# Optimization experiments

Measured on AMD Instinct MI355X. Metric: run time of the kernel, lower is better.

Reference implementation:

```python
import jax, jax.numpy as jnp
import numpy as np

B, C, H, W = 32, 512, 56, 56
GROUPS = 32
CG = C // GROUPS  # channels per group = 16
EPS = 1e-5


def setup_inputs() -> dict:
    key = jax.random.key(0)
    ks = jax.random.split(key, 5)
    return {
        "x": jax.random.normal(ks[0], (B, C, H, W), jnp.float32),
        "w1": jax.random.normal(ks[1], (CG, CG), jnp.float32) * 0.1,   # conv1x1 weight [out,in]
        "b1": jax.random.normal(ks[2], (CG,), jnp.float32) * 0.1,
        "w3": jax.random.normal(ks[3], (CG, CG, 3, 3), jnp.float32) * 0.05,  # conv3x3 OIHW
        "b3": jax.random.normal(ks[4], (CG,), jnp.float32) * 0.1,
        "gn_w": jnp.ones((CG,), jnp.float32),
        "gn_b": jnp.zeros((CG,), jnp.float32),
    }


def reference(x, w1, b1, w3, b3, gn_w, gn_b):
    b, c, h, w = x.shape
    bg = b * GROUPS
    gx = x.reshape(bg, CG, h, w)                                  # group_x
    # directional pooling
    x_h = gx.mean(axis=3, keepdims=True)                          # [bg,cg,h,1]
    x_w = gx.mean(axis=2, keepdims=True).transpose(0, 1, 3, 2)    # [bg,cg,w,1]
    y = jnp.concatenate([x_h, x_w], axis=2)                       # [bg,cg,h+w,1]
    # conv1x1 == channel mixing
    y = jnp.einsum('oc,bcld->bold', w1, y) + b1[None, :, None, None]
    xh = jax.nn.sigmoid(y[:, :, :h])                              # [bg,cg,h,1]
    xw = jax.nn.sigmoid(y[:, :, h:].transpose(0, 1, 3, 2))        # [bg,cg,1,w]
    # GroupNorm(num_groups=cg, num_channels=cg) == per-channel instance norm
    x1 = gx * xh * xw
    mu = x1.mean(axis=(2, 3), keepdims=True)
    var = x1.var(axis=(2, 3), keepdims=True)
    x1 = (x1 - mu) * jax.lax.rsqrt(var + EPS) * gn_w[None, :, None, None] + gn_b[None, :, None, None]
    # conv3x3 branch
    x2 = jax.lax.conv_general_dilated(
        gx, w3, (1, 1), 'SAME',
        dimension_numbers=('NCHW', 'OIHW', 'NCHW')) + b3[None, :, None, None]
    # cross attention weights
    a1 = jax.nn.softmax(x1.mean(axis=(2, 3)), axis=-1)            # [bg,cg]
    a2 = jax.nn.softmax(x2.mean(axis=(2, 3)), axis=-1)            # [bg,cg]
    x1f = x1.reshape(bg, CG, h * w)
    x2f = x2.reshape(bg, CG, h * w)
    out1 = jnp.einsum('bc,bcl->bl', a1, x2f)                      # [bg,hw]
    out2 = jnp.einsum('bc,bcl->bl', a2, x1f)                      # [bg,hw]
    weights = (out1 + out2).reshape(bg, 1, h, w)
    out = gx * jax.nn.sigmoid(weights)
    return out.reshape(b, c, h, w)
```

## Files before the change

### kernel.cpp

```cpp
#include <hip/hip_runtime.h>
#include <math.h>

#define GROUPS 32
#define CG 16
#define HH 56
#define WW 56
#define HW (HH*WW)
#define BG 1024
#define EPS 1e-5f

#define RB 4
#define NB 14
#define NR (RB+2)
#define LROW 60
#define CPAD 4
#define CSTR (NR*LROW+CPAD)
#define XWS 60
#define GHS 9

__global__ __launch_bounds__(256) void kA(const float* __restrict__ x,
        const float* __restrict__ w1, const float* __restrict__ b1,
        const float* __restrict__ w3, const float* __restrict__ b3,
        const float* __restrict__ gn_w, const float* __restrict__ gn_b,
        float* __restrict__ ws_xh, float* __restrict__ ws_xw,
        float* __restrict__ ws_asc, float* __restrict__ ws_aofs,
        float* __restrict__ ws_wa)
{
    const int g = blockIdx.x;
    const int tid = threadIdx.x;
    const float* gx = x + (size_t)g * CG * HW;

    __shared__ float s_row[CG][HH];
    __shared__ float s_col[CG][WW];
    __shared__ float s_xh[CG][HH];
    __shared__ float s_xw[CG][WW];
    __shared__ float s_st[CG][9];
    __shared__ float s_x2p[CG][CG];
    __shared__ float ls1[CG], ls2[CG];

    if (g == 0 && tid < CG * 9 + 1) {
        float m = gn_b[0];
        #pragma unroll
        for (int c = 1; c < CG; ++c) m = fmaxf(m, gn_b[c]);
        float a1[CG]; float den = 0.f;
        #pragma unroll
        for (int c = 0; c < CG; ++c) { a1[c] = __expf(gn_b[c] - m); den += a1[c]; }
        float inv = 1.f / den;
        if (tid < CG * 9) {
            int ci = tid / 9, k = tid - (tid / 9) * 9;
            float s = 0.f;
            #pragma unroll
            for (int o = 0; o < CG; ++o) s += a1[o] * w3[(size_t)(o * CG + ci) * 9 + k];
            ws_wa[tid] = s * inv;
        } else {
            float s = 0.f;
            #pragma unroll
            for (int o = 0; o < CG; ++o) s += a1[o] * b3[o];
            ws_wa[CG * 9] = s * inv;
        }
    }

    {
        const int grp = tid >> 4;
        const int q   = tid & 15;
        const float* pc = gx + grp * HW;
        float c0 = 0.f, c1 = 0.f, c2 = 0.f, c3 = 0.f;
        #pragma unroll 4
        for (int row = 0; row < HH; ++row) {
            float4 v = make_float4(0.f, 0.f, 0.f, 0.f);
            if (q < 14) v = *(const float4*)(pc + row * WW + q * 4);
            c0 += v.x; c1 += v.y; c2 += v.z; c3 += v.w;
            float rs = (v.x + v.y) + (v.z + v.w);
            rs += __shfl_down(rs, 8);
            rs += __shfl_down(rs, 4);
            rs += __shfl_down(rs, 2);
            rs += __shfl_down(rs, 1);
            if (q == 0) s_row[grp][row] = rs * (1.0f / WW);
        }
        if (q < 14) {
            s_col[grp][q * 4 + 0] = c0 * (1.0f / HH);
            s_col[grp][q * 4 + 1] = c1 * (1.0f / HH);
            s_col[grp][q * 4 + 2] = c2 * (1.0f / HH);
            s_col[grp][q * 4 + 3] = c3 * (1.0f / HH);
        }
    }
    __syncthreads();

    for (int t = tid; t < 2 * CG * HH; t += 256) {
        int hpart = (t < CG * HH);
        int tt = hpart ? t : t - CG * HH;
        int o = tt / HH, i = tt - (tt / HH) * HH;
        float v = b1[o];
        #pragma unroll
        for (int c = 0; c < CG; ++c)
            v += w1[o * CG + c] * (hpart ? s_row[c][i] : s_col[c][i]);
        float sg = 1.f / (1.f + __expf(-v));
        if (hpart) { s_xh[o][i] = sg; ws_xh[(size_t)g * CG * HH + tt] = sg; }
        else       { s_xw[o][i] = sg; ws_xw[(size_t)g * CG * WW + tt] = sg; }
    }

    if (tid < CG) {
        const int c = tid;
        float S = 0.f;
        #pragma unroll
        for (int r = 0; r < HH; ++r) S += s_row[c][r];
        s_st[c][0] = S * (float)WW;
        s_st[c][1] = (float)WW * s_row[c][HH - 1];
        s_st[c][2] = (float)WW * s_row[c][0];
        s_st[c][3] = (float)HH * s_col[c][WW - 1];
        s_st[c][4] = (float)HH * s_col[c][0];
        const float* p = gx + c * HW;
        s_st[c][5] = p[0];
        s_st[c][6] = p[WW - 1];
        s_st[c][7] = p[(HH - 1) * WW];
        s_st[c][8] = p[(HH - 1) * WW + WW - 1];
    }
    __syncthreads();

    {
        const int o = tid >> 4, c = tid & 15;
        const float* wp = w3 + (size_t)(o * CG + c) * 9;
        const float* st = s_st[c];
        float S = st[0];
        float acc = 0.f;
        #pragma unroll
        for (int dy = 0; dy < 3; ++dy) {
            float Rv = (dy == 0) ? st[1] : (dy == 2 ? st[2] : 0.f);
            #pragma unroll
            for (int dx = 0; dx < 3; ++dx) {
                float Cv = (dx == 0) ? st[3] : (dx == 2 ? st[4] : 0.f);
                float T = S - Rv - Cv;
                if (dy != 1 && dx != 1)
                    T += (dy == 0) ? ((dx == 0) ? st[8] : st[7])
                                   : ((dx == 0) ? st[6] : st[5]);
                acc += wp[dy * 3 + dx] * T;
            }
        }
        s_x2p[c][o] = acc;
    }

    {
        const int c = tid >> 4;
        const int q = tid & 15;
        float s1 = 0.f, s2 = 0.f;
        if (q < 14) {
            const float* pc = gx + c * HW;
            float xw0 = s_xw[c][q * 4 + 0], xw1 = s_xw[c][q * 4 + 1];
            float xw2 = s_xw[c][q * 4 + 2], xw3v = s_xw[c][q * 4 + 3];
            #pragma unroll 4
            for (int row = 0; row < HH; ++row) {
                float4 v = *(const float4*)(pc + row * WW + q * 4);
                float xh = s_xh[c][row];
                float t0 = v.x * xh * xw0;
                float t1 = v.y * xh * xw1;
                float t2 = v.z * xh * xw2;
                float t3 = v.w * xh * xw3v;
                s1 += (t0 + t1) + (t2 + t3);
                s2 += (t0 * t0 + t1 * t1) + (t2 * t2 + t3 * t3);
            }
        }
        s1 += __shfl_down(s1, 8);  s2 += __shfl_down(s2, 8);
        s1 += __shfl_down(s1, 4);  s2 += __shfl_down(s2, 4);
        s1 += __shfl_down(s1, 2);  s2 += __shfl_down(s2, 2);
        s1 += __shfl_down(s1, 1);  s2 += __shfl_down(s2, 1);
        if (q == 0) { ls1[c] = s1; ls2[c] = s2; }
    }
    __syncthreads();

    if (tid < CG) {
        const int o = tid;
        float x2 = (float)HW * b3[o];
        #pragma unroll
        for (int c = 0; c < CG; ++c) x2 += s_x2p[c][o];

        float mu  = ls1[o] * (1.0f / HW);
        float var = ls2[o] * (1.0f / HW) - mu * mu;
        float sc  = gn_w[o] * rsqrtf(var + EPS);
        float sh  = gn_b[o] - mu * sc;

        float v2 = x2 * (1.0f / HW);
        float m = v2;
        #pragma unroll
        for (int off = 8; off; off >>= 1) m = fmaxf(m, __shfl_xor(m, off));
        float e = __expf(v2 - m);
        float den = e;
        #pragma unroll
        for (int off = 8; off; off >>= 1) den += __shfl_xor(den, off);
        float a2 = e / den;

        ws_asc[(size_t)g * CG + o] = a2 * sc;
        float part = a2 * sh;
        #pragma unroll
        for (int off = 8; off; off >>= 1) part += __shfl_xor(part, off);
        if (o == 0) ws_aofs[g] = part;
    }
}

__global__ __launch_bounds__(256, 4) void kBC(const float* __restrict__ x,
        const float* __restrict__ ws_xh, const float* __restrict__ ws_xw,
        const float* __restrict__ ws_asc, const float* __restrict__ ws_aofs,
        const float* __restrict__ ws_wa, float* __restrict__ out)
{
    const int g = blockIdx.x / NB;
    const int band = blockIdx.x - g * NB;
    const int y0 = band * RB;
    const int tid = threadIdx.x;
    const float* gx = x + (size_t)g * CG * HW;
    float* og = out + (size_t)g * CG * HW;

    __shared__ float s_in[CG * CSTR];
    __shared__ float s_xw[CG * XWS];
    __shared__ float s_gh[CG * GHS];
    __shared__ float s_wa[CG * 9];
    __shared__ float s_bias;

    if (tid < 96) {
        int c = tid / NR, r = tid - c * NR;
        *(float4*)&s_in[c * CSTR + r * LROW] = make_float4(0.f, 0.f, 0.f, 0.f);
    } else if (tid < 112) {
        int c = tid - 96;
        *(float4*)&s_in[c * CSTR + NR * LROW] = make_float4(0.f, 0.f, 0.f, 0.f);
    } else {
        s_wa[tid - 112] = ws_wa[tid - 112];
    }
    if (tid < CG * 14) {
        int c = tid / 14, q = tid - c * 14;
        *(float4*)&s_xw[c * XWS + 4 * q] =
            *(const float4*)&ws_xw[(size_t)g * CG * WW + c * WW + 4 * q];
    }
    if (tid < CG * RB) {
        int c = tid >> 2, r = tid & 3;
        s_gh[c * GHS + r] = ws_asc[(size_t)g * CG + c]
                          * ws_xh[(size_t)g * CG * HH + c * HH + y0 + r];
    }
    if (tid == 255) s_bias = ws_wa[CG * 9] + ws_aofs[0 + g];

    for (int t = tid; t < CG * NR * (WW / 4); t += 256) {
        int c = t / (NR * 14);
        int rem = t - c * (NR * 14);
        int r = rem / 14, q = rem - r * 14;
        int ry = y0 - 1 + r;
        float4 v = make_float4(0.f, 0.f, 0.f, 0.f);
        if (ry >= 0 && ry < HH)
            v = *(const float4*)(gx + c * HW + ry * WW + 4 * q);
        *(float4*)&s_in[c * CSTR + r * LROW + 4 + 4 * q] = v;
    }
    __syncthreads();

    if (tid < 224) {
        const int c   = tid & 15;
        const int sp  = tid >> 4;
        const int ypr = sp / 7;
        const int k   = sp - ypr * 7;
        const int x0  = 8 * k;

        float w[9];
        #pragma unroll
        for (int i = 0; i < 9; ++i) w[i] = s_wa[c * 9 + i];

        float4 X0 = *(const float4*)&s_xw[c * XWS + x0];
        float4 X1 = *(const float4*)&s_xw[c * XWS + x0 + 4];
        float gh0 = s_gh[c * GHS + 2 * ypr];
        float gh1 = s_gh[c * GHS + 2 * ypr + 1];
        float g0[8], g1[8];
        {
            float xwv[8] = {X0.x, X0.y, X0.z, X0.w, X1.x, X1.y, X1.z, X1.w};
            #pragma unroll
            for (int j = 0; j < 8; ++j) { g0[j] = gh0 * xwv[j]; g1[j] = gh1 * xwv[j]; }
        }

        float acc0[8], acc1[8];
        #pragma unroll
        for (int j = 0; j < 8; ++j) { acc0[j] = 0.f; acc1[j] = 0.f; }

        const int base = c * CSTR + 2 * ypr * LROW + x0;
        #pragma unroll
        for (int rr = 0; rr < 4; ++rr) {
            const float* rp = &s_in[base + rr * LROW];
            float4 R0 = *(const float4*)(rp);
            float4 R1 = *(const float4*)(rp + 4);
            float4 R2 = *(const float4*)(rp + 8);
            float4 R3 = *(const float4*)(rp + 12);
            float win[10] = {R0.w, R1.x, R1.y, R1.z, R1.w,
                             R2.x, R2.y, R2.z, R2.w, R3.x};
            if (rr < 3) {
                float a0 = w[3 * rr], a1 = w[3 * rr + 1], a2 = w[3 * rr + 2];
                #pragma unroll
                for (int j = 0; j < 8; ++j)
                    acc0[j] += a0 * win[j] + a1 * win[j + 1] + a2 * win[j + 2];
            }
            if (rr > 0) {
                float b0 = w[3 * (rr - 1)], b1 = w[3 * (rr - 1) + 1], b2 = w[3 * (rr - 1) + 2];
                #pragma unroll
                for (int j = 0; j < 8; ++j)
                    acc1[j] += b0 * win[j] + b1 * win[j + 1] + b2 * win[j + 2];
            }
            if (rr == 1) {
                #pragma unroll
                for (int j = 0; j < 8; ++j) acc0[j] += g0[j] * win[j + 1];
            }
            if (rr == 2) {
                #pragma unroll
                for (int j = 0; j < 8; ++j) acc1[j] += g1[j] * win[j + 1];
            }
        }

        #pragma unroll
        for (int m = 1; m <= 8; m <<= 1) {
            #pragma unroll
            for (int j = 0; j < 8; ++j) {
                acc0[j] += __shfl_xor(acc0[j], m);
                acc1[j] += __shfl_xor(acc1[j], m);
            }
        }

        float bias = s_bias;
        float sg0[8], sg1[8];
        #pragma unroll
        for (int j = 0; j < 8; ++j) {
            sg0[j] = 1.f / (1.f + __expf(-(acc0[j] + bias)));
            sg1[j] = 1.f / (1.f + __expf(-(acc1[j] + bias)));
        }

        const float* c0p = &s_in[base + 1 * LROW + 4];
        const float* c1p = &s_in[base + 2 * LROW + 4];
        float4 C00 = *(const float4*)(c0p);
        float4 C01 = *(const float4*)(c0p + 4);
        float4 C10 = *(const float4*)(c1p);
        float4 C11 = *(const float4*)(c1p + 4);

        float* o0 = og + c * HW + (y0 + 2 * ypr) * WW + x0;
        float* o1 = o0 + WW;
        *(float4*)(o0)     = make_float4(C00.x * sg0[0], C00.y * sg0[1],
                                         C00.z * sg0[2], C00.w * sg0[3]);
        *(float4*)(o0 + 4) = make_float4(C01.x * sg0[4], C01.y * sg0[5],
                                         C01.z * sg0[6], C01.w * sg0[7]);
        *(float4*)(o1)     = make_float4(C10.x * sg1[0], C10.y * sg1[1],
                                         C10.z * sg1[2], C10.w * sg1[3]);
        *(float4*)(o1 + 4) = make_float4(C11.x * sg1[4], C11.y * sg1[5],
                                         C11.z * sg1[6], C11.w * sg1[7]);
    }
}

extern "C" void kernel_launch(void* const* d_in, const int* in_sizes, int n_in,
                              void* d_out, int out_size, void* d_ws, size_t ws_size,
                              hipStream_t stream)
{
    const float* x    = (const float*)d_in[0];
    const float* w1   = (const float*)d_in[1];
    const float* b1   = (const float*)d_in[2];
    const float* w3   = (const float*)d_in[3];
    const float* b3   = (const float*)d_in[4];
    const float* gn_w = (const float*)d_in[5];
    const float* gn_b = (const float*)d_in[6];
    float* out = (float*)d_out;

    float* ws = (float*)d_ws;
    float* ws_xh   = ws;
    float* ws_xw   = ws_xh + (size_t)BG * CG * HH;
    float* ws_asc  = ws_xw + (size_t)BG * CG * WW;
    float* ws_aofs = ws_asc + (size_t)BG * CG;
    float* ws_wa   = ws_aofs + (size_t)BG;

    kA<<<BG, 256, 0, stream>>>(x, w1, b1, w3, b3, gn_w, gn_b,
                               ws_xh, ws_xw, ws_asc, ws_aofs, ws_wa);
    kBC<<<BG * NB, 256, 0, stream>>>(x, ws_xh, ws_xw, ws_asc, ws_aofs,
                                     ws_wa, out);
}
```

Measured before the change: 486.4 us.

## Fuse stats and output kernels into one block-per-group kernel looping over bands

Merges the statistics kernel and the banded conv/gating kernel into one kernel. Each block handles one group, keeps the pooled gates, attention scales and folded conv weights in shared memory, then loops over 14 row bands to produce the output. This removes the workspace round-trip and the second launch, and the group's re-read of x may hit cache. In exchange, the grid shrinks from about 14k blocks to 1024, and each band's load and compute are serialized by barriers with no overlap, which can hurt latency hiding.

Result: faster. 476.8 us (-2.0%).

```diff
diff --git a/kernel.cpp b/kernel.cpp
--- a/kernel.cpp
+++ b/kernel.cpp
@@ -16,29 +16,34 @@
 #define CPAD 4
 #define CSTR (NR*LROW+CPAD)
 #define XWS 60
-#define GHS 9
-
-__global__ __launch_bounds__(256) void kA(const float* __restrict__ x,
+#define XHS 57
+
+#define U_ROW 0
+#define U_COL 896
+#define U_ST  1792
+#define U_X2P 1936
+#define U_LS1 2192
+#define U_LS2 2208
+
+__global__ __launch_bounds__(256, 4) void kF(const float* __restrict__ x,
         const float* __restrict__ w1, const float* __restrict__ b1,
         const float* __restrict__ w3, const float* __restrict__ b3,
         const float* __restrict__ gn_w, const float* __restrict__ gn_b,
-        float* __restrict__ ws_xh, float* __restrict__ ws_xw,
-        float* __restrict__ ws_asc, float* __restrict__ ws_aofs,
-        float* __restrict__ ws_wa)
+        float* __restrict__ out)
 {
     const int g = blockIdx.x;
     const int tid = threadIdx.x;
     const float* gx = x + (size_t)g * CG * HW;
-
-    __shared__ float s_row[CG][HH];
-    __shared__ float s_col[CG][WW];
-    __shared__ float s_xh[CG][HH];
-    __shared__ float s_xw[CG][WW];
-    __shared__ float s_st[CG][9];
-    __shared__ float s_x2p[CG][CG];
-    __shared__ float ls1[CG], ls2[CG];
-
-    if (g == 0 && tid < CG * 9 + 1) {
+    float* og = out + (size_t)g * CG * HW;
+
+    __shared__ float s_u[CG * CSTR];
+    __shared__ float s_xh[CG * XHS];
+    __shared__ float s_xw[CG * XWS];
+    __shared__ float s_wa[CG * 9 + 1];
+    __shared__ float s_asc[CG];
+    __shared__ float s_bias;
+
+    if (tid < CG * 9 + 1) {
         float m = gn_b[0];
         #pragma unroll
         for (int c = 1; c < CG; ++c) m = fmaxf(m, gn_b[c]);
@@ -51,12 +56,12 @@
             float s = 0.f;
             #pragma unroll
             for (int o = 0; o < CG; ++o) s += a1[o] * w3[(size_t)(o * CG + ci) * 9 + k];
-            ws_wa[tid] = s * inv;
+            s_wa[tid] = s * inv;
         } else {
             float s = 0.f;
             #pragma unroll
             for (int o = 0; o < CG; ++o) s += a1[o] * b3[o];
-            ws_wa[CG * 9] = s * inv;
+            s_wa[CG * 9] = s * inv;
         }
     }
 
@@ -65,23 +70,32 @@
         const int q   = tid & 15;
         const float* pc = gx + grp * HW;
         float c0 = 0.f, c1 = 0.f, c2 = 0.f, c3 = 0.f;
-        #pragma unroll 4
-        for (int row = 0; row < HH; ++row) {
-            float4 v = make_float4(0.f, 0.f, 0.f, 0.f);
-            if (q < 14) v = *(const float4*)(pc + row * WW + q * 4);
-            c0 += v.x; c1 += v.y; c2 += v.z; c3 += v.w;
-            float rs = (v.x + v.y) + (v.z + v.w);
-            rs += __shfl_down(rs, 8);
-            rs += __shfl_down(rs, 4);
-            rs += __shfl_down(rs, 2);
-            rs += __shfl_down(rs, 1);
-            if (q == 0) s_row[grp][row] = rs * (1.0f / WW);
+        #pragma unroll 2
+        for (int row = 0; row < HH; row += 2) {
+            float4 va = make_float4(0.f, 0.f, 0.f, 0.f);
+            float4 vb = va;
+            if (q < 14) {
+                va = *(const float4*)(pc + row * WW + q * 4);
+                vb = *(const float4*)(pc + (row + 1) * WW + q * 4);
+            }
+            c0 += va.x + vb.x; c1 += va.y + vb.y;
+            c2 += va.z + vb.z; c3 += va.w + vb.w;
+            float ra = (va.x + va.y) + (va.z + va.w);
+            float rb = (vb.x + vb.y) + (vb.z + vb.w);
+            ra += __shfl_down(ra, 8);  rb += __shfl_down(rb, 8);
+            ra += __shfl_down(ra, 4);  rb += __shfl_down(rb, 4);
+            ra += __shfl_down(ra, 2);  rb += __shfl_down(rb, 2);
+            ra += __shfl_down(ra, 1);  rb += __shfl_down(rb, 1);
+            if (q == 0) {
+                s_u[U_ROW + grp * HH + row]     = ra * (1.0f / WW);
+                s_u[U_ROW + grp * HH + row + 1] = rb * (1.0f / WW);
+            }
         }
         if (q < 14) {
-            s_col[grp][q * 4 + 0] = c0 * (1.0f / HH);
-            s_col[grp][q * 4 + 1] = c1 * (1.0f / HH);
-            s_col[grp][q * 4 + 2] = c2 * (1.0f / HH);
-            s_col[grp][q * 4 + 3] = c3 * (1.0f / HH);
+            s_u[U_COL + grp * WW + q * 4 + 0] = c0 * (1.0f / HH);
+            s_u[U_COL + grp * WW + q * 4 + 1] = c1 * (1.0f / HH);
+            s_u[U_COL + grp * WW + q * 4 + 2] = c2 * (1.0f / HH);
+            s_u[U_COL + grp * WW + q * 4 + 3] = c3 * (1.0f / HH);
         }
     }
     __syncthreads();
@@ -93,34 +107,36 @@
         float v = b1[o];
         #pragma unroll
         for (int c = 0; c < CG; ++c)
-            v += w1[o * CG + c] * (hpart ? s_row[c][i] : s_col[c][i]);
+            v += w1[o * CG + c] * (hpart ? s_u[U_ROW + c * HH + i]
+                                         : s_u[U_COL + c * WW + i]);
         float sg = 1.f / (1.f + __expf(-v));
-        if (hpart) { s_xh[o][i] = sg; ws_xh[(size_t)g * CG * HH + tt] = sg; }
-        else       { s_xw[o][i] = sg; ws_xw[(size_t)g * CG * WW + tt] = sg; }
+        if (hpart) s_xh[o * XHS + i] = sg;
+        else       s_xw[o * XWS + i] = sg;
     }
 
     if (tid < CG) {
         const int c = tid;
         float S = 0.f;
         #pragma unroll
-        for (int r = 0; r < HH; ++r) S += s_row[c][r];
-        s_st[c][0] = S * (float)WW;
-        s_st[c][1] = (float)WW * s_row[c][HH - 1];
-        s_st[c][2] = (float)WW * s_row[c][0];
-        s_st[c][3] = (float)HH * s_col[c][WW - 1];
-        s_st[c][4] = (float)HH * s_col[c][0];
+        for (int r = 0; r < HH; ++r) S += s_u[U_ROW + c * HH + r];
+        float* st = &s_u[U_ST + c * 9];
+        st[0] = S * (float)WW;
+        st[1] = (float)WW * s_u[U_ROW + c * HH + HH - 1];
+        st[2] = (float)WW * s_u[U_ROW + c * HH];
+        st[3] = (float)HH * s_u[U_COL + c * WW + WW - 1];
+        st[4] = (float)HH * s_u[U_COL + c * WW];
         const float* p = gx + c * HW;
-        s_st[c][5] = p[0];
-        s_st[c][6] = p[WW - 1];
-        s_st[c][7] = p[(HH - 1) * WW];
-        s_st[c][8] = p[(HH - 1) * WW + WW - 1];
+        st[5] = p[0];
+        st[6] = p[WW - 1];
+        st[7] = p[(HH - 1) * WW];
+        st[8] = p[(HH - 1) * WW + WW - 1];
     }
     __syncthreads();
 
     {
         const int o = tid >> 4, c = tid & 15;
         const float* wp = w3 + (size_t)(o * CG + c) * 9;
-        const float* st = s_st[c];
+        const float* st = &s_u[U_ST + c * 9];
         float S = st[0];
         float acc = 0.f;
         #pragma unroll
@@ -136,7 +152,7 @@
                 acc += wp[dy * 3 + dx] * T;
             }
         }
-        s_x2p[c][o] = acc;
+        s_u[U_X2P + c * CG + o] = acc;
     }
 
     {
@@ -145,12 +161,12 @@
         float s1 = 0.f, s2 = 0.f;
         if (q < 14) {
             const float* pc = gx + c * HW;
-            float xw0 = s_xw[c][q * 4 + 0], xw1 = s_xw[c][q * 4 + 1];
-            float xw2 = s_xw[c][q * 4 + 2], xw3v = s_xw[c][q * 4 + 3];
+            float xw0 = s_xw[c * XWS + q * 4 + 0], xw1 = s_xw[c * XWS + q * 4 + 1];
+            float xw2 = s_xw[c * XWS + q * 4 + 2], xw3v = s_xw[c * XWS + q * 4 + 3];
             #pragma unroll 4
             for (int row = 0; row < HH; ++row) {
                 float4 v = *(const float4*)(pc + row * WW + q * 4);
-                float xh = s_xh[c][row];
+                float xh = s_xh[c * XHS + row];
                 float t0 = v.x * xh * xw0;
                 float t1 = v.y * xh * xw1;
                 float t2 = v.z * xh * xw2;
@@ -163,7 +179,7 @@
         s1 += __shfl_down(s1, 4);  s2 += __shfl_down(s2, 4);
         s1 += __shfl_down(s1, 2);  s2 += __shfl_down(s2, 2);
         s1 += __shfl_down(s1, 1);  s2 += __shfl_down(s2, 1);
-        if (q == 0) { ls1[c] = s1; ls2[c] = s2; }
+        if (q == 0) { s_u[U_LS1 + c] = s1; s_u[U_LS2 + c] = s2; }
     }
     __syncthreads();
 
@@ -171,10 +187,10 @@
         const int o = tid;
         float x2 = (float)HW * b3[o];
         #pragma unroll
-        for (int c = 0; c < CG; ++c) x2 += s_x2p[c][o];
-
-        float mu  = ls1[o] * (1.0f / HW);
-        float var = ls2[o] * (1.0f / HW) - mu * mu;
+        for (int c = 0; c < CG; ++c) x2 += s_u[U_X2P + c * CG + o];
+
+        float mu  = s_u[U_LS1 + o] * (1.0f / HW);
+        float var = s_u[U_LS2 + o] * (1.0f / HW) - mu * mu;
         float sc  = gn_w[o] * rsqrtf(var + EPS);
         float sh  = gn_b[o] - mu * sc;
 
@@ -188,157 +204,137 @@
         for (int off = 8; off; off >>= 1) den += __shfl_xor(den, off);
         float a2 = e / den;
 
-        ws_asc[(size_t)g * CG + o] = a2 * sc;
+        s_asc[o] = a2 * sc;
         float part = a2 * sh;
         #pragma unroll
         for (int off = 8; off; off >>= 1) part += __shfl_xor(part, off);
-        if (o == 0) ws_aofs[g] = part;
-    }
-}
-
-__global__ __launch_bounds__(256, 4) void kBC(const float* __restrict__ x,
-        const float* __restrict__ ws_xh, const float* __restrict__ ws_xw,
-        const float* __restrict__ ws_asc, const float* __restrict__ ws_aofs,
-        const float* __restrict__ ws_wa, float* __restrict__ out)
-{
-    const int g = blockIdx.x / NB;
-    const int band = blockIdx.x - g * NB;
-    const int y0 = band * RB;
-    const int tid = threadIdx.x;
-    const float* gx = x + (size_t)g * CG * HW;
-    float* og = out + (size_t)g * CG * HW;
-
-    __shared__ float s_in[CG * CSTR];
-    __shared__ float s_xw[CG * XWS];
-    __shared__ float s_gh[CG * GHS];
-    __shared__ float s_wa[CG * 9];
-    __shared__ float s_bias;
+        if (o == 0) s_bias = part + s_wa[CG * 9];
+    }
+    __syncthreads();
 
     if (tid < 96) {
-        int c = tid / NR, r = tid - c * NR;
-        *(float4*)&s_in[c * CSTR + r * LROW] = make_float4(0.f, 0.f, 0.f, 0.f);
+        int c = tid / NR, r = tid - (tid / NR) * NR;
+        *(float4*)&s_u[c * CSTR + r * LROW] = make_float4(0.f, 0.f, 0.f, 0.f);
     } else if (tid < 112) {
         int c = tid - 96;
-        *(float4*)&s_in[c * CSTR + NR * LROW] = make_float4(0.f, 0.f, 0.f, 0.f);
-    } else {
-        s_wa[tid - 112] = ws_wa[tid - 112];
-    }
-    if (tid < CG * 14) {
-        int c = tid / 14, q = tid - c * 14;
-        *(float4*)&s_xw[c * XWS + 4 * q] =
-            *(const float4*)&ws_xw[(size_t)g * CG * WW + c * WW + 4 * q];
-    }
-    if (tid < CG * RB) {
-        int c = tid >> 2, r = tid & 3;
-        s_gh[c * GHS + r] = ws_asc[(size_t)g * CG + c]
-                          * ws_xh[(size_t)g * CG * HH + c * HH + y0 + r];
-    }
-    if (tid == 255) s_bias = ws_wa[CG * 9] + ws_aofs[0 + g];
-
-    for (int t = tid; t < CG * NR * (WW / 4); t += 256) {
-        int c = t / (NR * 14);
-        int rem = t - c * (NR * 14);
-        int r = rem / 14, q = rem - r * 14;
-        int ry = y0 - 1 + r;
-        float4 v = make_float4(0.f, 0.f, 0.f, 0.f);
-        if (ry >= 0 && ry < HH)
-            v = *(const float4*)(gx + c * HW + ry * WW + 4 * q);
-        *(float4*)&s_in[c * CSTR + r * LROW + 4 + 4 * q] = v;
-    }
-    __syncthreads();
-
+        *(float4*)&s_u[c * CSTR + NR * LROW] = make_float4(0.f, 0.f, 0.f, 0.f);
+    }
+    for (int t = tid; t < CG * HH; t += 256) {
+        int c = t / HH, y = t - (t / HH) * HH;
+        s_xh[c * XHS + y] *= s_asc[c];
+    }
+
+    int cc = 0, ypr = 0, x0 = 0;
+    float wreg[9];
+    float xwv[8];
     if (tid < 224) {
-        const int c   = tid & 15;
-        const int sp  = tid >> 4;
-        const int ypr = sp / 7;
-        const int k   = sp - ypr * 7;
-        const int x0  = 8 * k;
-
-        float w[9];
-        #pragma unroll
-        for (int i = 0; i < 9; ++i) w[i] = s_wa[c * 9 + i];
-
-        float4 X0 = *(const float4*)&s_xw[c * XWS + x0];
-        float4 X1 = *(const float4*)&s_xw[c * XWS + x0 + 4];
-        float gh0 = s_gh[c * GHS + 2 * ypr];
-        float gh1 = s_gh[c * GHS + 2 * ypr + 1];
-        float g0[8], g1[8];
-        {
-            float xwv[8] = {X0.x, X0.y, X0.z, X0.w, X1.x, X1.y, X1.z, X1.w};
+        cc  = tid & 15;
+        int sp = tid >> 4;
+        ypr = sp / 7;
+        x0  = (sp - ypr * 7) * 8;
+        #pragma unroll
+        for (int i = 0; i < 9; ++i) wreg[i] = s_wa[cc * 9 + i];
+        float4 X0 = *(const float4*)&s_xw[cc * XWS + x0];
+        float4 X1 = *(const float4*)&s_xw[cc * XWS + x0 + 4];
+        xwv[0] = X0.x; xwv[1] = X0.y; xwv[2] = X0.z; xwv[3] = X0.w;
+        xwv[4] = X1.x; xwv[5] = X1.y; xwv[6] = X1.z; xwv[7] = X1.w;
+    }
+
+    for (int band = 0; band < NB; ++band) {
+        const int y0 = band * RB;
+
+        for (int t = tid; t < CG * NR * 14; t += 256) {
+            int c = t / (NR * 14);
+            int rem = t - c * (NR * 14);
+            int r = rem / 14, q = rem - r * 14;
+            int ry = y0 - 1 + r;
+            float4 v = make_float4(0.f, 0.f, 0.f, 0.f);
+            if (ry >= 0 && ry < HH)
+                v = *(const float4*)(gx + c * HW + ry * WW + 4 * q);
+            *(float4*)&s_u[c * CSTR + r * LROW + 4 + 4 * q] = v;
+        }
+        __syncthreads();
+
+        if (tid < 224) {
+            float gh0 = s_xh[cc * XHS + y0 + 2 * ypr];
+            float gh1 = s_xh[cc * XHS + y0 + 2 * ypr + 1];
+            float g0[8], g1[8];
             #pragma unroll
             for (int j = 0; j < 8; ++j) { g0[j] = gh0 * xwv[j]; g1[j] = gh1 * xwv[j]; }
-        }
-
-        float acc0[8], acc1[8];
-        #pragma unroll
-        for (int j = 0; j < 8; ++j) { acc0[j] = 0.f; acc1[j] = 0.f; }
-
-        const int base = c * CSTR + 2 * ypr * LROW + x0;
-        #pragma unroll
-        for (int rr = 0; rr < 4; ++rr) {
-            const float* rp = &s_in[base + rr * LROW];
-            float4 R0 = *(const float4*)(rp);
-            float4 R1 = *(const float4*)(rp + 4);
-            float4 R2 = *(const float4*)(rp + 8);
-            float4 R3 = *(const float4*)(rp + 12);
-            float win[10] = {R0.w, R1.x, R1.y, R1.z, R1.w,
-                             R2.x, R2.y, R2.z, R2.w, R3.x};
-            if (rr < 3) {
-                float a0 = w[3 * rr], a1 = w[3 * rr + 1], a2 = w[3 * rr + 2];
+
+            float acc0[8], acc1[8];
+            #pragma unroll
+            for (int j = 0; j < 8; ++j) { acc0[j] = 0.f; acc1[j] = 0.f; }
+
+            const int base = cc * CSTR + 2 * ypr * LROW + x0;
+            #pragma unroll
+            for (int rr = 0; rr < 4; ++rr) {
+                const float* rp = &s_u[base + rr * LROW];
+                float4 R0 = *(const float4*)(rp);
+                float4 R1 = *(const float4*)(rp + 4);
+                float4 R2 = *(const float4*)(rp + 8);
+                float4 R3 = *(const float4*)(rp + 12);
+                float win[10] = {R0.w, R1.x, R1.y, R1.z, R1.w,
+                                 R2.x, R2.y, R2.z, R2.w, R3.x};
+                if (rr < 3) {
+                    float a0 = wreg[3 * rr], a1 = wreg[3 * rr + 1], a2 = wreg[3 * rr + 2];
+                    #pragma unroll
+                    for (int j = 0; j < 8; ++j)
+                        acc0[j] += a0 * win[j] + a1 * win[j + 1] + a2 * win[j + 2];
+                }
+                if (rr > 0) {
+                    float b0 = wreg[3 * (rr - 1)], b1v = wreg[3 * (rr - 1) + 1],
+                          b2 = wreg[3 * (rr - 1) + 2];
+                    #pragma unroll
+                    for (int j = 0; j < 8; ++j)
+                        acc1[j] += b0 * win[j] + b1v * win[j + 1] + b2 * win[j + 2];
+                }
+                if (rr == 1) {
+                    #pragma unroll
+                    for (int j = 0; j < 8; ++j) acc0[j] += g0[j] * win[j + 1];
+                }
+                if (rr == 2) {
+                    #pragma unroll
+                    for (int j = 0; j < 8; ++j) acc1[j] += g1[j] * win[j + 1];
+                }
+            }
+
+            #pragma unroll
+            for (int m = 1; m <= 8; m <<= 1) {
                 #pragma unroll
-                for (int j = 0; j < 8; ++j)
-                    acc0[j] += a0 * win[j] + a1 * win[j + 1] + a2 * win[j + 2];
-            }
-            if (rr > 0) {
-                float b0 = w[3 * (rr - 1)], b1 = w[3 * (rr - 1) + 1], b2 = w[3 * (rr - 1) + 2];
-                #pragma unroll
-                for (int j = 0; j < 8; ++j)
-                    acc1[j] += b0 * win[j] + b1 * win[j + 1] + b2 * win[j + 2];
-            }
-            if (rr == 1) {
-                #pragma unroll
-                for (int j = 0; j < 8; ++j) acc0[j] += g0[j] * win[j + 1];
-            }
-            if (rr == 2) {
-                #pragma unroll
-                for (int j = 0; j < 8; ++j) acc1[j] += g1[j] * win[j + 1];
-            }
-        }
-
-        #pragma unroll
-        for (int m = 1; m <= 8; m <<= 1) {
+                for (int j = 0; j < 8; ++j) {
+                    acc0[j] += __shfl_xor(acc0[j], m);
+                    acc1[j] += __shfl_xor(acc1[j], m);
+                }
+            }
+
+            float bias = s_bias;
+            float sg0[8], sg1[8];
             #pragma unroll
             for (int j = 0; j < 8; ++j) {
-                acc0[j] += __shfl_xor(acc0[j], m);
-                acc1[j] += __shfl_xor(acc1[j], m);
-            }
-        }
-
-        float bias = s_bias;
-        float sg0[8], sg1[8];
-        #pragma unroll
-        for (int j = 0; j < 8; ++j) {
-            sg0[j] = 1.f / (1.f + __expf(-(acc0[j] + bias)));
-            sg1[j] = 1.f / (1.f + __expf(-(acc1[j] + bias)));
-        }
-
-        const float* c0p = &s_in[base + 1 * LROW + 4];
-        const float* c1p = &s_in[base + 2 * LROW + 4];
-        float4 C00 = *(const float4*)(c0p);
-        float4 C01 = *(const float4*)(c0p + 4);
-        float4 C10 = *(const float4*)(c1p);
-        float4 C11 = *(const float4*)(c1p + 4);
-
-        float* o0 = og + c * HW + (y0 + 2 * ypr) * WW + x0;
-        float* o1 = o0 + WW;
-        *(float4*)(o0)     = make_float4(C00.x * sg0[0], C00.y * sg0[1],
-                                         C00.z * sg0[2], C00.w * sg0[3]);
-        *(float4*)(o0 + 4) = make_float4(C01.x * sg0[4], C01.y * sg0[5],
-                                         C01.z * sg0[6], C01.w * sg0[7]);
-        *(float4*)(o1)     = make_float4(C10.x * sg1[0], C10.y * sg1[1],
-                                         C10.z * sg1[2], C10.w * sg1[3]);
-        *(float4*)(o1 + 4) = make_float4(C11.x * sg1[4], C11.y * sg1[5],
-                                         C11.z * sg1[6], C11.w * sg1[7]);
+                sg0[j] = 1.f / (1.f + __expf(-(acc0[j] + bias)));
+                sg1[j] = 1.f / (1.f + __expf(-(acc1[j] + bias)));
+            }
+
+            const float* c0p = &s_u[base + 1 * LROW + 4];
+            const float* c1p = &s_u[base + 2 * LROW + 4];
+            float4 C00 = *(const float4*)(c0p);
+            float4 C01 = *(const float4*)(c0p + 4);
+            float4 C10 = *(const float4*)(c1p);
+            float4 C11 = *(const float4*)(c1p + 4);
+
+            float* o0 = og + cc * HW + (y0 + 2 * ypr) * WW + x0;
+            float* o1 = o0 + WW;
+            *(float4*)(o0)     = make_float4(C00.x * sg0[0], C00.y * sg0[1],
+                                             C00.z * sg0[2], C00.w * sg0[3]);
+            *(float4*)(o0 + 4) = make_float4(C01.x * sg0[4], C01.y * sg0[5],
+                                             C01.z * sg0[6], C01.w * sg0[7]);
+            *(float4*)(o1)     = make_float4(C10.x * sg1[0], C10.y * sg1[1],
+                                             C10.z * sg1[2], C10.w * sg1[3]);
+            *(float4*)(o1 + 4) = make_float4(C11.x * sg1[4], C11.y * sg1[5],
+                                             C11.z * sg1[6], C11.w * sg1[7]);
+        }
+        __syncthreads();
     }
 }
 
@@ -354,16 +350,7 @@
     const float* gn_w = (const float*)d_in[5];
     const float* gn_b = (const float*)d_in[6];
     float* out = (float*)d_out;
-
-    float* ws = (float*)d_ws;
-    float* ws_xh   = ws;
-    float* ws_xw   = ws_xh + (size_t)BG * CG * HH;
-    float* ws_asc  = ws_xw + (size_t)BG * CG * WW;
-    float* ws_aofs = ws_asc + (size_t)BG * CG;
-    float* ws_wa   = ws_aofs + (size_t)BG;
-
-    kA<<<BG, 256, 0, stream>>>(x, w1, b1, w3, b3, gn_w, gn_b,
-                               ws_xh, ws_xw, ws_asc, ws_aofs, ws_wa);
-    kBC<<<BG * NB, 256, 0, stream>>>(x, ws_xh, ws_xw, ws_asc, ws_aofs,
-                                     ws_wa, out);
+    (void)d_ws; (void)ws_size;
+
+    kF<<<BG, 256, 0, stream>>>(x, w1, b1, w3, b3, gn_w, gn_b, out);
 }
```
